# Kernel optimization log

Measured on AMD Instinct MI355X. Metric: run time of the kernel, lower is better.

## Reference

```python
import jax, jax.numpy as jnp
import numpy as np

BN_EPS = 1e-5

def setup_inputs() -> dict:
    key = jax.random.key(0)
    ks = jax.random.split(key, 6)
    B, C, N = 8, 256, 4096
    da = C // 4
    return {
        "x": jax.random.normal(ks[0], (B, C, N), dtype=jnp.float32),
        "Wq": jax.random.normal(ks[1], (da, C), dtype=jnp.float32) * (C ** -0.5),
        "Wk": jax.random.normal(ks[2], (da, C), dtype=jnp.float32) * (C ** -0.5),
        "Wv": jax.random.normal(ks[3], (C, C), dtype=jnp.float32) * (C ** -0.5),
        "Wp": jax.random.normal(ks[4], (C, C), dtype=jnp.float32) * (C ** -0.5),
        "bn_gamma": jnp.ones((C,), dtype=jnp.float32),
        "bn_beta": jnp.zeros((C,), dtype=jnp.float32),
        "bn_mean": jnp.zeros((C,), dtype=jnp.float32),
        "bn_var": jnp.ones((C,), dtype=jnp.float32),
    }

def reference(x, Wq, Wk, Wv, Wp, bn_gamma, bn_beta, bn_mean, bn_var):
    # x: [B, C, N]; 1x1 Conv1d == channel matmul
    q = jnp.einsum('bcn,dc->bnd', x, Wq)          # [B, N, da]
    k = jnp.einsum('bcn,dc->bdn', x, Wk)          # [B, da, N]
    v = jnp.einsum('bcn,dc->bnd', x, Wv)          # [B, N, C]
    energy = jnp.einsum('bnd,bdm->bnm', q, k)     # [B, N, N]
    # offset-attention double normalization: softmax over dim=1 (rows), then L1 over dim=-1
    attn = jax.nn.softmax(energy, axis=1)
    attn = attn / (1e-9 + attn.sum(axis=-1, keepdims=True))
    fsa = jnp.einsum('bnm,bmc->bcn', attn, v)     # [B, C, N]
    y = x - fsa
    h = jnp.einsum('bcn,dc->bdn', y, Wp)          # 1x1 conv of LBR
    # BatchNorm1d (inference-mode with running stats)
    inv = bn_gamma / jnp.sqrt(bn_var + BN_EPS)
    h = h * inv[None, :, None] + (bn_beta - bn_mean * inv)[None, :, None]
    return jax.nn.relu(h) + x
```

## Files before the change

### kernel.cpp

```cpp
#include <hip/hip_runtime.h>
#include <math.h>

#define BD 8
#define CD 256
#define ND 4096
#define DA 64

typedef __attribute__((ext_vector_type(8))) short short8v;
typedef __attribute__((ext_vector_type(4))) float float4v;

static __device__ __forceinline__ float4v mfma16(short8v a, short8v b, float4v c) {
  return __builtin_amdgcn_mfma_f32_16x16x32_bf16(a, b, c, 0, 0, 0);
}
static __device__ __forceinline__ unsigned short f2bf(float f) {
  union { float f; unsigned int u; } v; v.f = f;
  return (unsigned short)((v.u + 0x7fffu + ((v.u >> 16) & 1u)) >> 16);
}
static __device__ __forceinline__ float bf2f(unsigned short h) {
  union { unsigned int u; float f; } v; v.u = (unsigned int)h << 16;
  return v.f;
}
static __device__ __forceinline__ int sw(int row, int c8) {
  return row * 64 + (((c8) ^ (row & 7)) << 3);
}
typedef const __attribute__((address_space(1))) unsigned int g_u32;
typedef __attribute__((address_space(3))) unsigned int l_u32;
static __device__ __forceinline__ void gld16(const void* g, void* l) {
  __builtin_amdgcn_global_load_lds((g_u32*)g, (l_u32*)l, 16, 0, 0);
}

__global__ __launch_bounds__(256) void k_prep(const float* __restrict__ x,
                                              unsigned short* __restrict__ xTh,
                                              unsigned short* __restrict__ xTl) {
  const int n0 = blockIdx.x * 64, c0 = blockIdx.y * 64, b = blockIdx.z;
  __shared__ float Xs[64][68];
  const int tid = threadIdx.x;
  const int r0 = tid >> 4, col4 = (tid & 15) * 4;
#pragma unroll
  for (int j = 0; j < 4; ++j) {
    int r = r0 + j * 16;
    *(float4*)&Xs[r][col4] =
        *(const float4*)&x[((size_t)(b * CD + c0 + r)) * ND + n0 + col4];
  }
  __syncthreads();
  const int n = tid >> 2, cg = (tid & 3) * 16;
  unsigned short h[16], l[16];
#pragma unroll
  for (int j = 0; j < 16; ++j) {
    float v = Xs[cg + j][n];
    h[j] = f2bf(v);
    l[j] = f2bf(v - bf2f(h[j]));
  }
  size_t o = ((size_t)b * ND + n0 + n) * CD + c0 + cg;
#pragma unroll
  for (int j = 0; j < 4; ++j) {
    *(ushort4*)&xTh[o + j * 4] = *(ushort4*)&h[j * 4];
    *(ushort4*)&xTl[o + j * 4] = *(ushort4*)&l[j * 4];
  }
}

__global__ void k_prepW(const float* __restrict__ Wq, const float* __restrict__ Wk,
                        const float* __restrict__ Wv, const float* __restrict__ Wp,
                        unsigned short* Wch, unsigned short* Wcl,
                        unsigned short* Wph, unsigned short* Wpl) {
  int i = blockIdx.x * 256 + threadIdx.x;
  int row = i >> 6, c4 = (i & 63) * 4;
  const float* src; unsigned short *dh, *dl; int r, drow;
  if (row < 64)       { src = Wq; r = row;       dh = Wch; dl = Wcl; drow = row; }
  else if (row < 128) { src = Wk; r = row - 64;  dh = Wch; dl = Wcl; drow = row; }
  else if (row < 384) { src = Wv; r = row - 128; dh = Wch; dl = Wcl; drow = row; }
  else                { src = Wp; r = row - 384; dh = Wph; dl = Wpl; drow = row - 384; }
  float4 f = *(const float4*)&src[(size_t)r * 256 + c4];
  ushort4 hh, ll;
  hh.x = f2bf(f.x); hh.y = f2bf(f.y); hh.z = f2bf(f.z); hh.w = f2bf(f.w);
  ll.x = f2bf(f.x - bf2f(hh.x)); ll.y = f2bf(f.y - bf2f(hh.y));
  ll.z = f2bf(f.z - bf2f(hh.z)); ll.w = f2bf(f.w - bf2f(hh.w));
  *(ushort4*)&dh[(size_t)drow * 256 + c4] = hh;
  *(ushort4*)&dl[(size_t)drow * 256 + c4] = ll;
}

__global__ __launch_bounds__(512) void k_proj(
    const unsigned short* __restrict__ xTh, const unsigned short* __restrict__ xTl,
    const unsigned short* __restrict__ Wch, const unsigned short* __restrict__ Wcl,
    unsigned short* __restrict__ qh, unsigned short* __restrict__ kh,
    unsigned short* __restrict__ kl, unsigned short* __restrict__ vT) {
  const int n0 = blockIdx.x * 128, b = blockIdx.y;
  const int tid = threadIdx.x, w = tid >> 6, lane = tid & 63, lq = lane & 15,
            quad = lane >> 4;
  __shared__ __align__(16) unsigned short xs[2][2][128][40];
  float4v O[24];
#pragma unroll
  for (int t = 0; t < 24; ++t) O[t] = (float4v){0.f, 0.f, 0.f, 0.f};

  const int srow = tid >> 2, sc4 = tid & 3;
  uint4 rh, rl;
  auto load_slice = [&](int ks) {
    size_t a = ((size_t)b * ND + n0 + srow) * CD + ks * 32 + sc4 * 8;
    rh = *(const uint4*)(xTh + a);
    rl = *(const uint4*)(xTl + a);
  };
  auto write_slice = [&](int buf) {
    *(uint4*)&xs[buf][0][srow][sc4 * 8] = rh;
    *(uint4*)&xs[buf][1][srow][sc4 * 8] = rl;
  };
  load_slice(0); write_slice(0);
#pragma unroll 1
  for (int ks = 0; ks < 8; ++ks) {
    __syncthreads();
    if (ks < 7) load_slice(ks + 1);
    short8v bxh = *(const short8v*)&xs[ks & 1][0][w * 16 + lq][quad * 8];
    short8v bxl = *(const short8v*)&xs[ks & 1][1][w * 16 + lq][quad * 8];
#pragma unroll
    for (int t = 0; t < 24; ++t) {
      size_t a = (size_t)(t * 16 + lq) * CD + ks * 32 + quad * 8;
      short8v awh = *(const short8v*)(Wch + a);
      short8v awl = *(const short8v*)(Wcl + a);
      O[t] = mfma16(awh, bxh, O[t]);
      O[t] = mfma16(awl, bxh, O[t]);
      O[t] = mfma16(awh, bxl, O[t]);
    }
    if (ks < 7) write_slice((ks + 1) & 1);
  }
  const int n = n0 + w * 16 + lq;
#pragma unroll
  for (int t = 0; t < 24; ++t) {
    if (t < 4) {
      ushort4 hh;
      hh.x = f2bf(O[t][0]); hh.y = f2bf(O[t][1]);
      hh.z = f2bf(O[t][2]); hh.w = f2bf(O[t][3]);
      *(ushort4*)&qh[((size_t)b * ND + n) * DA + t * 16 + quad * 4] = hh;
    } else if (t < 8) {
      ushort4 hh, ll;
      hh.x = f2bf(O[t][0]); hh.y = f2bf(O[t][1]);
      hh.z = f2bf(O[t][2]); hh.w = f2bf(O[t][3]);
      ll.x = f2bf(O[t][0] - bf2f(hh.x)); ll.y = f2bf(O[t][1] - bf2f(hh.y));
      ll.z = f2bf(O[t][2] - bf2f(hh.z)); ll.w = f2bf(O[t][3] - bf2f(hh.w));
      size_t o = ((size_t)b * ND + n) * DA + (t - 4) * 16 + quad * 4;
      *(ushort4*)&kh[o] = hh;
      *(ushort4*)&kl[o] = ll;
    } else {
#pragma unroll
      for (int r = 0; r < 4; ++r) {
        int c = (t - 8) * 16 + quad * 4 + r;
        vT[((size_t)b * CD + c) * ND + n] = f2bf(O[t][r]);
      }
    }
  }
}

__global__ __launch_bounds__(512, 4) void k_colsum(
    const unsigned short* __restrict__ qh, const unsigned short* __restrict__ khp,
    const unsigned short* __restrict__ klp, float* __restrict__ Dp) {
  const int bid = blockIdx.x, b = bid & 7, half = (bid >> 3) & 1,
            m0 = (bid >> 4) * 128;
  const int nbase = half * 2048;
  const int tid = threadIdx.x, w = tid >> 6, lane = tid & 63, lq = lane & 15,
            quad = lane >> 4;
  const int mq = w & 3, nh = w >> 2;
  __shared__ __align__(16) unsigned short qbuf[3][4096];
  __shared__ float Cb[128];
  short8v bkh[2][2], bkl[2][2];
#pragma unroll
  for (int sub = 0; sub < 2; ++sub)
#pragma unroll
    for (int k = 0; k < 2; ++k) {
      size_t a = ((size_t)b * ND + m0 + mq * 32 + sub * 16 + lq) * DA + k * 32 + quad * 8;
      bkh[sub][k] = *(const short8v*)(khp + a);
      bkl[sub][k] = *(const short8v*)(klp + a);
    }
  const int srow = w * 8 + (lane >> 3), sck = lane & 7;
  auto stageQ = [&](int it, int qn) {
    const unsigned short* src = qh + ((size_t)b * ND + nbase + it * 64 + srow) * DA +
                                ((sck ^ (srow & 7)) << 3);
    gld16(src, &qbuf[qn][0] + (size_t)w * 512);
  };
  stageQ(0, 0);
  stageQ(1, 1);
  asm volatile("s_waitcnt vmcnt(1)\n\ts_barrier" ::: "memory");
  float cs0 = 0.f, cs1 = 0.f;
  int rc = 0, sc = 2;
#pragma unroll 1
  for (int i = 0; i < 32; ++i) {
    if (i < 30) { stageQ(i + 2, sc); sc = (sc + 1 == 3) ? 0 : sc + 1; }
#pragma unroll
    for (int s = 0; s < 2; ++s) {
      short8v ah[2];
#pragma unroll
      for (int k = 0; k < 2; ++k)
        ah[k] = *(const short8v*)&qbuf[rc][sw(nh * 32 + s * 16 + lq, k * 4 + quad)];
#pragma unroll
      for (int sub = 0; sub < 2; ++sub) {
        float4v acc = {0.f, 0.f, 0.f, 0.f};
#pragma unroll
        for (int k = 0; k < 2; ++k) {
          acc = mfma16(ah[k], bkh[sub][k], acc);
          acc = mfma16(ah[k], bkl[sub][k], acc);
        }
        float e0 = __expf(acc[0]) + __expf(acc[1]) + __expf(acc[2]) + __expf(acc[3]);
        if (sub == 0) cs0 += e0; else cs1 += e0;
      }
    }
    rc = (rc + 1 == 3) ? 0 : rc + 1;
    if (i < 30)
      asm volatile("s_waitcnt vmcnt(1) lgkmcnt(0)\n\ts_barrier" ::: "memory");
    else
      asm volatile("s_waitcnt vmcnt(0) lgkmcnt(0)\n\ts_barrier" ::: "memory");
  }
  cs0 += __shfl_down(cs0, 16); cs0 += __shfl_down(cs0, 32);
  cs1 += __shfl_down(cs1, 16); cs1 += __shfl_down(cs1, 32);
  if (nh == 0 && lane < 16) {
    Cb[mq * 32 + lane] = cs0;
    Cb[mq * 32 + 16 + lane] = cs1;
  }
  __syncthreads();
  if (nh == 1 && lane < 16) {
    float t0 = Cb[mq * 32 + lane] + cs0;
    float t1 = Cb[mq * 32 + 16 + lane] + cs1;
    size_t o = (size_t)half * (BD * ND) + (size_t)b * ND + m0 + mq * 32 + lane;
    Dp[o] = t0;
    Dp[o + 16] = t1;
  }
}

__global__ void k_rcp(const float* __restrict__ Dp, float* __restrict__ Drec) {
  int i = blockIdx.x * 256 + threadIdx.x;
  float4 a = *(const float4*)&Dp[(size_t)i * 4];
  float4 c = *(const float4*)&Dp[(size_t)(BD * ND) + (size_t)i * 4];
  float4 r;
  r.x = 1.f / (a.x + c.x); r.y = 1.f / (a.y + c.y);
  r.z = 1.f / (a.z + c.z); r.w = 1.f / (a.w + c.w);
  *(float4*)&Drec[(size_t)i * 4] = r;
}

__global__ __launch_bounds__(512, 2) void k_attn(
    const unsigned short* __restrict__ qh, const unsigned short* __restrict__ khp,
    const unsigned short* __restrict__ klp, const unsigned short* __restrict__ vT,
    const float* __restrict__ Drec, unsigned short* xhy,
    const unsigned short* __restrict__ xTl) {
  const int bid = blockIdx.x, b = bid & 7, n0 = (bid >> 3) * 128;
  const int tid = threadIdx.x, w = tid >> 6, lane = tid & 63, lq = lane & 15,
            quad = lane >> 4;
  const int nq = w & 3, ch = w >> 2;
  __shared__ __align__(16) unsigned short vbuf[3][16384];
  __shared__ __align__(16) unsigned short Pb[2][8192];
  __shared__ float Sb[128];

  short8v aq[2][2];
#pragma unroll
  for (int s = 0; s < 2; ++s)
#pragma unroll
    for (int k = 0; k < 2; ++k)
      aq[s][k] = *(const short8v*)(qh + ((size_t)b * ND + n0 + nq * 32 + s * 16 + lq) * DA +
                                   k * 32 + quad * 8);
  float4v O[2][8];
#pragma unroll
  for (int s = 0; s < 2; ++s)
#pragma unroll
    for (int t = 0; t < 8; ++t) O[s][t] = (float4v){0.f, 0.f, 0.f, 0.f};
  float rs[2] = {0.f, 0.f};

  auto stageV = [&](int mt, int vn) {
    unsigned short* base = &vbuf[vn][0];
#pragma unroll
    for (int j = 0; j < 4; ++j) {
      int cidx = tid + j * 512;
      int row = cidx >> 3, ckpos = cidx & 7;
      const unsigned short* src =
          vT + ((size_t)b * CD + row) * ND + mt * 64 + ((ckpos ^ (row & 7)) << 3);
      gld16(src, base + (size_t)(w * 64 + j * 512) * 8);
    }
  };
  short8v kc[8], kn[8];
  auto kload = [&](short8v* dst, int mt) {
#pragma unroll
    for (int sub = 0; sub < 2; ++sub)
#pragma unroll
      for (int k = 0; k < 2; ++k) {
        size_t a = ((size_t)b * ND + mt * 64 + ch * 32 + sub * 16 + lq) * DA +
                   k * 32 + quad * 8;
        dst[sub * 4 + k * 2 + 0] = *(const short8v*)(khp + a);
        dst[sub * 4 + k * 2 + 1] = *(const short8v*)(klp + a);
      }
  };
  auto doPV = [&](const unsigned short* Pc, const unsigned short* vc) {
    short8v ap[2][2];
#pragma unroll
    for (int s = 0; s < 2; ++s)
#pragma unroll
      for (int k = 0; k < 2; ++k)
        ap[s][k] = *(const short8v*)&Pc[sw(nq * 32 + s * 16 + lq, k * 4 + quad)];
#pragma unroll
    for (int t = 0; t < 8; ++t) {
      const int trow = (ch * 8 + t) * 16 + lq;
#pragma unroll
      for (int k = 0; k < 2; ++k) {
        short8v bv = *(const short8v*)&vc[sw(trow, k * 4 + quad)];
#pragma unroll
        for (int s = 0; s < 2; ++s) O[s][t] = mfma16(bv, ap[s][k], O[s][t]);
      }
    }
  };

  float4 drc4[2], drn4[2];
  stageV(0, 0);
  kload(kc, 0);
#pragma unroll
  for (int sub = 0; sub < 2; ++sub)
    drc4[sub] = *(const float4*)&Drec[(size_t)b * ND + ch * 32 + sub * 16 + quad * 4];

  int vs = 1, vp = 0;
#pragma unroll 1
  for (int i = 0; i < 64; ++i) {
    if (i > 0) {
      doPV(&Pb[(i - 1) & 1][0], &vbuf[vp][0]);
      vp = (vp + 1 == 3) ? 0 : vp + 1;
    }
    if (i < 63) {
      kload(kn, i + 1);
#pragma unroll
      for (int sub = 0; sub < 2; ++sub)
        drn4[sub] = *(const float4*)&Drec[(size_t)b * ND + (i + 1) * 64 + ch * 32 +
                                          sub * 16 + quad * 4];
      stageV(i + 1, vs);
      vs = (vs + 1 == 3) ? 0 : vs + 1;
    }
    unsigned short* Pcur = &Pb[i & 1][0];
#pragma unroll
    for (int sub = 0; sub < 2; ++sub) {
#pragma unroll
      for (int s = 0; s < 2; ++s) {
        float4v acc = {0.f, 0.f, 0.f, 0.f};
#pragma unroll
        for (int k = 0; k < 2; ++k) {
          acc = mfma16(kc[sub * 4 + k * 2 + 0], aq[s][k], acc);
          acc = mfma16(kc[sub * 4 + k * 2 + 1], aq[s][k], acc);
        }
        float p0 = __expf(acc[0]) * drc4[sub].x;
        float p1 = __expf(acc[1]) * drc4[sub].y;
        float p2 = __expf(acc[2]) * drc4[sub].z;
        float p3 = __expf(acc[3]) * drc4[sub].w;
        rs[s] += (p0 + p1) + (p2 + p3);
        unsigned int w0 =
            (__float_as_uint(p0) >> 16) | (__float_as_uint(p1) & 0xffff0000u);
        unsigned int w1 =
            (__float_as_uint(p2) >> 16) | (__float_as_uint(p3) & 0xffff0000u);
        const int nl = nq * 32 + s * 16 + lq;
        const int c8 = ch * 4 + sub * 2 + (quad >> 1);
        uint2 wv; wv.x = w0; wv.y = w1;
        *(uint2*)&Pcur[nl * 64 + ((c8 ^ (nl & 7)) << 3) + ((quad & 1) << 2)] = wv;
      }
    }
    if (i < 63) {
#pragma unroll
      for (int t = 0; t < 8; ++t) kc[t] = kn[t];
      drc4[0] = drn4[0]; drc4[1] = drn4[1];
    }
    if (i < 63)
      asm volatile("s_waitcnt vmcnt(4) lgkmcnt(0)\n\ts_barrier" ::: "memory");
    else
      asm volatile("s_waitcnt vmcnt(0) lgkmcnt(0)\n\ts_barrier" ::: "memory");
  }
  doPV(&Pb[1][0], &vbuf[vp][0]);

  rs[0] += __shfl_xor(rs[0], 16); rs[0] += __shfl_xor(rs[0], 32);
  rs[1] += __shfl_xor(rs[1], 16); rs[1] += __shfl_xor(rs[1], 32);
  if (ch == 0 && lane < 16) {
    Sb[nq * 32 + lane] = rs[0];
    Sb[nq * 32 + 16 + lane] = rs[1];
  }
  __syncthreads();
  if (ch == 1 && lane < 16) {
    Sb[nq * 32 + lane] += rs[0];
    Sb[nq * 32 + 16 + lane] += rs[1];
  }
  __syncthreads();
  float rsc[2];
#pragma unroll
  for (int s = 0; s < 2; ++s)
    rsc[s] = 1.0f / (1e-9f + Sb[nq * 32 + s * 16 + lq]);
#pragma unroll
  for (int t = 0; t < 8; ++t) {
    const int cb = (ch * 8 + t) * 16 + quad * 4;
#pragma unroll
    for (int s = 0; s < 2; ++s) {
      const int n = n0 + nq * 32 + s * 16 + lq;
      const size_t off = ((size_t)b * ND + n) * CD + cb;
      ushort4 h4 = *(const ushort4*)&xhy[off];
      ushort4 l4 = *(const ushort4*)&xTl[off];
      ushort4 o4;
      o4.x = f2bf(bf2f(h4.x) + bf2f(l4.x) - O[s][t][0] * rsc[s]);
      o4.y = f2bf(bf2f(h4.y) + bf2f(l4.y) - O[s][t][1] * rsc[s]);
      o4.z = f2bf(bf2f(h4.z) + bf2f(l4.z) - O[s][t][2] * rsc[s]);
      o4.w = f2bf(bf2f(h4.w) + bf2f(l4.w) - O[s][t][3] * rsc[s]);
      *(ushort4*)&xhy[off] = o4;
    }
  }
}

__global__ __launch_bounds__(256) void k_final(const unsigned short* __restrict__ y,
                                               const unsigned short* __restrict__ Wpb,
                                               const float* __restrict__ x,
                                               const float* __restrict__ gamma,
                                               const float* __restrict__ beta,
                                               const float* __restrict__ mean,
                                               const float* __restrict__ var,
                                               float* __restrict__ out) {
  const int bid = blockIdx.x;
  const int b = bid & 7;
  const int rem = bid >> 3;
  const int n0 = (rem & 63) * 64;
  const int d0 = (rem >> 6) * 64;
  const int tid = threadIdx.x;
  const int wave = tid >> 6, lane = tid & 63, lq = lane & 15, quad = lane >> 4;
  const int dw = d0 + wave * 16;
  float4v O[4];
#pragma unroll
  for (int s = 0; s < 4; ++s) O[s] = (float4v){0.f, 0.f, 0.f, 0.f};
#pragma unroll
  for (int chh = 0; chh < 8; ++chh) {
    const size_t ab = (size_t)(dw + lq) * CD + chh * 32 + quad * 8;
    short8v a0 = *(const short8v*)(Wpb + ab);
#pragma unroll
    for (int s = 0; s < 4; ++s) {
      const size_t bb = ((size_t)b * ND + n0 + s * 16 + lq) * CD + chh * 32 + quad * 8;
      short8v bv = *(const short8v*)(y + bb);
      O[s] = mfma16(a0, bv, O[s]);
    }
  }
#pragma unroll
  for (int r = 0; r < 4; ++r) {
    const int d = dw + quad * 4 + r;
    const float inv  = gamma[d] / sqrtf(var[d] + 1e-5f);
    const float bias = beta[d] - mean[d] * inv;
#pragma unroll
    for (int s = 0; s < 4; ++s) {
      const int n = n0 + s * 16 + lq;
      const size_t oi = ((size_t)b * CD + d) * ND + n;
      out[oi] = fmaxf(O[s][r] * inv + bias, 0.f) + x[oi];
    }
  }
}

extern "C" void kernel_launch(void* const* d_in, const int* in_sizes, int n_in,
                              void* d_out, int out_size, void* d_ws, size_t ws_size,
                              hipStream_t stream) {
  const float* x     = (const float*)d_in[0];
  const float* Wq    = (const float*)d_in[1];
  const float* Wk    = (const float*)d_in[2];
  const float* Wv    = (const float*)d_in[3];
  const float* Wp    = (const float*)d_in[4];
  const float* gamma = (const float*)d_in[5];
  const float* beta  = (const float*)d_in[6];
  const float* mean  = (const float*)d_in[7];
  const float* var   = (const float*)d_in[8];
  float* out = (float*)d_out;

  char* wsp = (char*)d_ws;
  unsigned short* qhp = (unsigned short*)wsp; wsp += (size_t)BD * ND * DA * 2;
  unsigned short* khp = (unsigned short*)wsp; wsp += (size_t)BD * ND * DA * 2;
  unsigned short* klp = (unsigned short*)wsp; wsp += (size_t)BD * ND * DA * 2;
  unsigned short* vT  = (unsigned short*)wsp; wsp += (size_t)BD * CD * ND * 2;
  unsigned short* xTh = (unsigned short*)wsp; wsp += (size_t)BD * ND * CD * 2;
  unsigned short* xTl = (unsigned short*)wsp; wsp += (size_t)BD * ND * CD * 2;
  unsigned short* Wch = (unsigned short*)wsp; wsp += (size_t)384 * 256 * 2;
  unsigned short* Wcl = (unsigned short*)wsp; wsp += (size_t)384 * 256 * 2;
  unsigned short* Wph = (unsigned short*)wsp; wsp += (size_t)256 * 256 * 2;
  unsigned short* Wpl = (unsigned short*)wsp; wsp += (size_t)256 * 256 * 2;
  float* Drec = (float*)wsp; wsp += (size_t)BD * ND * 4;
  float* Dp   = (float*)wsp; wsp += (size_t)2 * BD * ND * 4;
  unsigned short* y = xTh;

  dim3 blk(256), blk5(512);
  k_prep<<<dim3(ND / 64, CD / 64, BD), blk, 0, stream>>>(x, xTh, xTl);
  k_prepW<<<dim3(160), blk, 0, stream>>>(Wq, Wk, Wv, Wp, Wch, Wcl, Wph, Wpl);
  k_proj<<<dim3(ND / 128, BD), blk5, 0, stream>>>(xTh, xTl, Wch, Wcl, qhp, khp,
                                                  klp, vT);
  k_colsum<<<dim3(512), blk5, 0, stream>>>(qhp, khp, klp, Dp);
  k_rcp<<<dim3(32), blk, 0, stream>>>(Dp, Drec);
  k_attn<<<dim3(256), blk5, 0, stream>>>(qhp, khp, klp, vT, Drec, y, xTl);
  k_final<<<dim3(2048), blk, 0, stream>>>(y, Wph, x, gamma, beta, mean, var, out);
}
```

Measured before the change: 512.0 us.

## Materialize exp-energy matrix in halves and run separate PV GEMM

The old code computed the energy matrix twice: once for column sums and once inside the fused attention kernel. The new code computes exp(energy) once per half of the key dimension and stores it as a bf16 P matrix in global memory, writing column sums at the same time. A second pass takes reciprocals of those column sums and folds them into V in place. A separate GEMM kernel then computes P·V and the row sums, and accumulates partial results across the two halves through an fp32 buffer. This removes the recomputed QK products but adds a large write and read of P through HBM, plus extra kernel launches.

```diff
diff --git a/kernel.cpp b/kernel.cpp
--- a/kernel.cpp
+++ b/kernel.cpp
@@ -5,6 +5,8 @@
 #define CD 256
 #define ND 4096
 #define DA 64
+#define HM 2048
+#define OSTR 260
 
 typedef __attribute__((ext_vector_type(8))) short short8v;
 typedef __attribute__((ext_vector_type(4))) float float4v;
@@ -148,16 +150,19 @@
   }
 }
 
-__global__ __launch_bounds__(512, 4) void k_colsum(
+__global__ __launch_bounds__(512, 4) void k_expE(
     const unsigned short* __restrict__ qh, const unsigned short* __restrict__ khp,
-    const unsigned short* __restrict__ klp, float* __restrict__ Dp) {
-  const int bid = blockIdx.x, b = bid & 7, half = (bid >> 3) & 1,
-            m0 = (bid >> 4) * 128;
-  const int nbase = half * 2048;
+    const unsigned short* __restrict__ klp, unsigned short* __restrict__ P,
+    float* __restrict__ Dp, int mhalf) {
+  const int mtile = blockIdx.x, nq4 = blockIdx.y, b = blockIdx.z;
+  const int m0 = mhalf * HM + mtile * 128;
+  const int mmb = mtile * 128;
+  const int nbase = nq4 * 1024;
   const int tid = threadIdx.x, w = tid >> 6, lane = tid & 63, lq = lane & 15,
             quad = lane >> 4;
   const int mq = w & 3, nh = w >> 2;
-  __shared__ __align__(16) unsigned short qbuf[3][4096];
+  __shared__ __align__(16) unsigned short qbuf[2][4096];
+  __shared__ __align__(16) unsigned short Et[64][136];
   __shared__ float Cb[128];
   short8v bkh[2][2], bkl[2][2];
 #pragma unroll
@@ -168,232 +173,262 @@
       bkh[sub][k] = *(const short8v*)(khp + a);
       bkl[sub][k] = *(const short8v*)(klp + a);
     }
-  const int srow = w * 8 + (lane >> 3), sck = lane & 7;
-  auto stageQ = [&](int it, int qn) {
+  const int srow = tid >> 3, sck = tid & 7;
+  auto stageQ = [&](int it, int buf) {
     const unsigned short* src = qh + ((size_t)b * ND + nbase + it * 64 + srow) * DA +
                                 ((sck ^ (srow & 7)) << 3);
-    gld16(src, &qbuf[qn][0] + (size_t)w * 512);
+    gld16(src, &qbuf[buf][0] + (size_t)w * 512);
   };
+  float cs[2][4] = {{0.f, 0.f, 0.f, 0.f}, {0.f, 0.f, 0.f, 0.f}};
   stageQ(0, 0);
-  stageQ(1, 1);
-  asm volatile("s_waitcnt vmcnt(1)\n\ts_barrier" ::: "memory");
-  float cs0 = 0.f, cs1 = 0.f;
-  int rc = 0, sc = 2;
+  asm volatile("s_waitcnt vmcnt(0)\n\ts_barrier" ::: "memory");
 #pragma unroll 1
-  for (int i = 0; i < 32; ++i) {
-    if (i < 30) { stageQ(i + 2, sc); sc = (sc + 1 == 3) ? 0 : sc + 1; }
+  for (int i = 0; i < 16; ++i) {
+    if (i < 15) stageQ(i + 1, (i + 1) & 1);
 #pragma unroll
     for (int s = 0; s < 2; ++s) {
       short8v ah[2];
 #pragma unroll
       for (int k = 0; k < 2; ++k)
-        ah[k] = *(const short8v*)&qbuf[rc][sw(nh * 32 + s * 16 + lq, k * 4 + quad)];
+        ah[k] = *(const short8v*)&qbuf[i & 1][sw(nh * 32 + s * 16 + lq, k * 4 + quad)];
 #pragma unroll
       for (int sub = 0; sub < 2; ++sub) {
         float4v acc = {0.f, 0.f, 0.f, 0.f};
 #pragma unroll
         for (int k = 0; k < 2; ++k) {
-          acc = mfma16(ah[k], bkh[sub][k], acc);
-          acc = mfma16(ah[k], bkl[sub][k], acc);
+          acc = mfma16(bkh[sub][k], ah[k], acc);
+          acc = mfma16(bkl[sub][k], ah[k], acc);
         }
-        float e0 = __expf(acc[0]) + __expf(acc[1]) + __expf(acc[2]) + __expf(acc[3]);
-        if (sub == 0) cs0 += e0; else cs1 += e0;
-      }
-    }
-    rc = (rc + 1 == 3) ? 0 : rc + 1;
-    if (i < 30)
-      asm volatile("s_waitcnt vmcnt(1) lgkmcnt(0)\n\ts_barrier" ::: "memory");
-    else
-      asm volatile("s_waitcnt vmcnt(0) lgkmcnt(0)\n\ts_barrier" ::: "memory");
-  }
-  cs0 += __shfl_down(cs0, 16); cs0 += __shfl_down(cs0, 32);
-  cs1 += __shfl_down(cs1, 16); cs1 += __shfl_down(cs1, 32);
-  if (nh == 0 && lane < 16) {
-    Cb[mq * 32 + lane] = cs0;
-    Cb[mq * 32 + 16 + lane] = cs1;
-  }
-  __syncthreads();
-  if (nh == 1 && lane < 16) {
-    float t0 = Cb[mq * 32 + lane] + cs0;
-    float t1 = Cb[mq * 32 + 16 + lane] + cs1;
-    size_t o = (size_t)half * (BD * ND) + (size_t)b * ND + m0 + mq * 32 + lane;
-    Dp[o] = t0;
-    Dp[o + 16] = t1;
-  }
-}
-
-__global__ void k_rcp(const float* __restrict__ Dp, float* __restrict__ Drec) {
-  int i = blockIdx.x * 256 + threadIdx.x;
-  float4 a = *(const float4*)&Dp[(size_t)i * 4];
-  float4 c = *(const float4*)&Dp[(size_t)(BD * ND) + (size_t)i * 4];
-  float4 r;
-  r.x = 1.f / (a.x + c.x); r.y = 1.f / (a.y + c.y);
-  r.z = 1.f / (a.z + c.z); r.w = 1.f / (a.w + c.w);
-  *(float4*)&Drec[(size_t)i * 4] = r;
-}
-
-__global__ __launch_bounds__(512, 2) void k_attn(
-    const unsigned short* __restrict__ qh, const unsigned short* __restrict__ khp,
-    const unsigned short* __restrict__ klp, const unsigned short* __restrict__ vT,
-    const float* __restrict__ Drec, unsigned short* xhy,
-    const unsigned short* __restrict__ xTl) {
-  const int bid = blockIdx.x, b = bid & 7, n0 = (bid >> 3) * 128;
-  const int tid = threadIdx.x, w = tid >> 6, lane = tid & 63, lq = lane & 15,
-            quad = lane >> 4;
-  const int nq = w & 3, ch = w >> 2;
-  __shared__ __align__(16) unsigned short vbuf[3][16384];
-  __shared__ __align__(16) unsigned short Pb[2][8192];
-  __shared__ float Sb[128];
-
-  short8v aq[2][2];
-#pragma unroll
-  for (int s = 0; s < 2; ++s)
-#pragma unroll
-    for (int k = 0; k < 2; ++k)
-      aq[s][k] = *(const short8v*)(qh + ((size_t)b * ND + n0 + nq * 32 + s * 16 + lq) * DA +
-                                   k * 32 + quad * 8);
-  float4v O[2][8];
-#pragma unroll
-  for (int s = 0; s < 2; ++s)
-#pragma unroll
-    for (int t = 0; t < 8; ++t) O[s][t] = (float4v){0.f, 0.f, 0.f, 0.f};
-  float rs[2] = {0.f, 0.f};
-
-  auto stageV = [&](int mt, int vn) {
-    unsigned short* base = &vbuf[vn][0];
-#pragma unroll
-    for (int j = 0; j < 4; ++j) {
-      int cidx = tid + j * 512;
-      int row = cidx >> 3, ckpos = cidx & 7;
-      const unsigned short* src =
-          vT + ((size_t)b * CD + row) * ND + mt * 64 + ((ckpos ^ (row & 7)) << 3);
-      gld16(src, base + (size_t)(w * 64 + j * 512) * 8);
-    }
-  };
-  short8v kc[8], kn[8];
-  auto kload = [&](short8v* dst, int mt) {
-#pragma unroll
-    for (int sub = 0; sub < 2; ++sub)
-#pragma unroll
-      for (int k = 0; k < 2; ++k) {
-        size_t a = ((size_t)b * ND + mt * 64 + ch * 32 + sub * 16 + lq) * DA +
-                   k * 32 + quad * 8;
-        dst[sub * 4 + k * 2 + 0] = *(const short8v*)(khp + a);
-        dst[sub * 4 + k * 2 + 1] = *(const short8v*)(klp + a);
-      }
-  };
-  auto doPV = [&](const unsigned short* Pc, const unsigned short* vc) {
-    short8v ap[2][2];
-#pragma unroll
-    for (int s = 0; s < 2; ++s)
-#pragma unroll
-      for (int k = 0; k < 2; ++k)
-        ap[s][k] = *(const short8v*)&Pc[sw(nq * 32 + s * 16 + lq, k * 4 + quad)];
-#pragma unroll
-    for (int t = 0; t < 8; ++t) {
-      const int trow = (ch * 8 + t) * 16 + lq;
-#pragma unroll
-      for (int k = 0; k < 2; ++k) {
-        short8v bv = *(const short8v*)&vc[sw(trow, k * 4 + quad)];
-#pragma unroll
-        for (int s = 0; s < 2; ++s) O[s][t] = mfma16(bv, ap[s][k], O[s][t]);
-      }
-    }
-  };
-
-  float4 drc4[2], drn4[2];
-  stageV(0, 0);
-  kload(kc, 0);
-#pragma unroll
-  for (int sub = 0; sub < 2; ++sub)
-    drc4[sub] = *(const float4*)&Drec[(size_t)b * ND + ch * 32 + sub * 16 + quad * 4];
-
-  int vs = 1, vp = 0;
-#pragma unroll 1
-  for (int i = 0; i < 64; ++i) {
-    if (i > 0) {
-      doPV(&Pb[(i - 1) & 1][0], &vbuf[vp][0]);
-      vp = (vp + 1 == 3) ? 0 : vp + 1;
-    }
-    if (i < 63) {
-      kload(kn, i + 1);
-#pragma unroll
-      for (int sub = 0; sub < 2; ++sub)
-        drn4[sub] = *(const float4*)&Drec[(size_t)b * ND + (i + 1) * 64 + ch * 32 +
-                                          sub * 16 + quad * 4];
-      stageV(i + 1, vs);
-      vs = (vs + 1 == 3) ? 0 : vs + 1;
-    }
-    unsigned short* Pcur = &Pb[i & 1][0];
-#pragma unroll
-    for (int sub = 0; sub < 2; ++sub) {
-#pragma unroll
-      for (int s = 0; s < 2; ++s) {
-        float4v acc = {0.f, 0.f, 0.f, 0.f};
-#pragma unroll
-        for (int k = 0; k < 2; ++k) {
-          acc = mfma16(kc[sub * 4 + k * 2 + 0], aq[s][k], acc);
-          acc = mfma16(kc[sub * 4 + k * 2 + 1], aq[s][k], acc);
-        }
-        float p0 = __expf(acc[0]) * drc4[sub].x;
-        float p1 = __expf(acc[1]) * drc4[sub].y;
-        float p2 = __expf(acc[2]) * drc4[sub].z;
-        float p3 = __expf(acc[3]) * drc4[sub].w;
-        rs[s] += (p0 + p1) + (p2 + p3);
+        float p0 = __expf(acc[0]), p1 = __expf(acc[1]);
+        float p2 = __expf(acc[2]), p3 = __expf(acc[3]);
+        cs[sub][0] += p0; cs[sub][1] += p1; cs[sub][2] += p2; cs[sub][3] += p3;
         unsigned int w0 =
             (__float_as_uint(p0) >> 16) | (__float_as_uint(p1) & 0xffff0000u);
         unsigned int w1 =
             (__float_as_uint(p2) >> 16) | (__float_as_uint(p3) & 0xffff0000u);
-        const int nl = nq * 32 + s * 16 + lq;
-        const int c8 = ch * 4 + sub * 2 + (quad >> 1);
+        const int nl = nh * 32 + s * 16 + lq;
         uint2 wv; wv.x = w0; wv.y = w1;
-        *(uint2*)&Pcur[nl * 64 + ((c8 ^ (nl & 7)) << 3) + ((quad & 1) << 2)] = wv;
+        *(uint2*)((unsigned short*)Et + nl * 136 + mq * 32 + sub * 16 + quad * 4) = wv;
       }
     }
-    if (i < 63) {
-#pragma unroll
-      for (int t = 0; t < 8; ++t) kc[t] = kn[t];
-      drc4[0] = drn4[0]; drc4[1] = drn4[1];
-    }
-    if (i < 63)
-      asm volatile("s_waitcnt vmcnt(4) lgkmcnt(0)\n\ts_barrier" ::: "memory");
-    else
-      asm volatile("s_waitcnt vmcnt(0) lgkmcnt(0)\n\ts_barrier" ::: "memory");
-  }
-  doPV(&Pb[1][0], &vbuf[vp][0]);
-
-  rs[0] += __shfl_xor(rs[0], 16); rs[0] += __shfl_xor(rs[0], 32);
-  rs[1] += __shfl_xor(rs[1], 16); rs[1] += __shfl_xor(rs[1], 32);
-  if (ch == 0 && lane < 16) {
-    Sb[nq * 32 + lane] = rs[0];
-    Sb[nq * 32 + 16 + lane] = rs[1];
+    asm volatile("s_waitcnt lgkmcnt(0)\n\ts_barrier" ::: "memory");
+    {
+      uint4 u0 = *(const uint4*)((const unsigned short*)Et + srow * 136 + sck * 16);
+      uint4 u1 = *(const uint4*)((const unsigned short*)Et + srow * 136 + sck * 16 + 8);
+      size_t po = ((size_t)b * ND + nbase + i * 64 + srow) * HM + mmb + sck * 16;
+      *(uint4*)(P + po) = u0;
+      *(uint4*)(P + po + 8) = u1;
+    }
+    asm volatile("s_waitcnt vmcnt(2) lgkmcnt(0)\n\ts_barrier" ::: "memory");
+  }
+#pragma unroll
+  for (int sub = 0; sub < 2; ++sub)
+#pragma unroll
+    for (int r = 0; r < 4; ++r) {
+      cs[sub][r] += __shfl_xor(cs[sub][r], 1);
+      cs[sub][r] += __shfl_xor(cs[sub][r], 2);
+      cs[sub][r] += __shfl_xor(cs[sub][r], 4);
+      cs[sub][r] += __shfl_xor(cs[sub][r], 8);
+    }
+  if (nh == 0 && lq == 0) {
+#pragma unroll
+    for (int sub = 0; sub < 2; ++sub) {
+      float4 v4; v4.x = cs[sub][0]; v4.y = cs[sub][1]; v4.z = cs[sub][2]; v4.w = cs[sub][3];
+      *(float4*)&Cb[mq * 32 + sub * 16 + quad * 4] = v4;
+    }
   }
   __syncthreads();
-  if (ch == 1 && lane < 16) {
-    Sb[nq * 32 + lane] += rs[0];
-    Sb[nq * 32 + 16 + lane] += rs[1];
-  }
-  __syncthreads();
-  float rsc[2];
-#pragma unroll
-  for (int s = 0; s < 2; ++s)
-    rsc[s] = 1.0f / (1e-9f + Sb[nq * 32 + s * 16 + lq]);
-#pragma unroll
-  for (int t = 0; t < 8; ++t) {
-    const int cb = (ch * 8 + t) * 16 + quad * 4;
-#pragma unroll
-    for (int s = 0; s < 2; ++s) {
-      const int n = n0 + nq * 32 + s * 16 + lq;
-      const size_t off = ((size_t)b * ND + n) * CD + cb;
-      ushort4 h4 = *(const ushort4*)&xhy[off];
-      ushort4 l4 = *(const ushort4*)&xTl[off];
-      ushort4 o4;
-      o4.x = f2bf(bf2f(h4.x) + bf2f(l4.x) - O[s][t][0] * rsc[s]);
-      o4.y = f2bf(bf2f(h4.y) + bf2f(l4.y) - O[s][t][1] * rsc[s]);
-      o4.z = f2bf(bf2f(h4.z) + bf2f(l4.z) - O[s][t][2] * rsc[s]);
-      o4.w = f2bf(bf2f(h4.w) + bf2f(l4.w) - O[s][t][3] * rsc[s]);
-      *(ushort4*)&xhy[off] = o4;
-    }
+  if (nh == 1 && lq == 0) {
+#pragma unroll
+    for (int sub = 0; sub < 2; ++sub) {
+      float4 v4 = *(const float4*)&Cb[mq * 32 + sub * 16 + quad * 4];
+      v4.x += cs[sub][0]; v4.y += cs[sub][1]; v4.z += cs[sub][2]; v4.w += cs[sub][3];
+      *(float4*)&Dp[((size_t)nq4 * 8 + b) * HM + mmb + mq * 32 + sub * 16 + quad * 4] = v4;
+    }
+  }
+}
+
+__global__ void k_rcp2(const float* __restrict__ Dp, float* __restrict__ drc,
+                       int mhalf) {
+  int i = blockIdx.x * 256 + threadIdx.x;
+  int b = i >> 9, mm = (i & 511) * 4;
+  float4 s0 = *(const float4*)&Dp[((size_t)0 * 8 + b) * HM + mm];
+  float4 s1 = *(const float4*)&Dp[((size_t)1 * 8 + b) * HM + mm];
+  float4 s2 = *(const float4*)&Dp[((size_t)2 * 8 + b) * HM + mm];
+  float4 s3 = *(const float4*)&Dp[((size_t)3 * 8 + b) * HM + mm];
+  float4 r;
+  r.x = 1.f / (s0.x + s1.x + s2.x + s3.x);
+  r.y = 1.f / (s0.y + s1.y + s2.y + s3.y);
+  r.z = 1.f / (s0.z + s1.z + s2.z + s3.z);
+  r.w = 1.f / (s0.w + s1.w + s2.w + s3.w);
+  *(float4*)&drc[(size_t)b * ND + mhalf * HM + mm] = r;
+}
+
+__global__ void k_vext(unsigned short* __restrict__ vT,
+                       const float* __restrict__ drc, int mhalf) {
+  int idx = blockIdx.x * 256 + threadIdx.x;
+  int m8 = idx & 255, c = (idx >> 8) & 255, b = idx >> 16;
+  const int mb = mhalf * HM + m8 * 8;
+  size_t va = ((size_t)(b * CD + c)) * ND + mb;
+  short8v v = *(const short8v*)(vT + va);
+  float4 d0 = *(const float4*)&drc[(size_t)b * ND + mb];
+  float4 d1 = *(const float4*)&drc[(size_t)b * ND + mb + 4];
+  ushort4 o0, o1;
+  o0.x = f2bf(bf2f((unsigned short)v[0]) * d0.x);
+  o0.y = f2bf(bf2f((unsigned short)v[1]) * d0.y);
+  o0.z = f2bf(bf2f((unsigned short)v[2]) * d0.z);
+  o0.w = f2bf(bf2f((unsigned short)v[3]) * d0.w);
+  o1.x = f2bf(bf2f((unsigned short)v[4]) * d1.x);
+  o1.y = f2bf(bf2f((unsigned short)v[5]) * d1.y);
+  o1.z = f2bf(bf2f((unsigned short)v[6]) * d1.z);
+  o1.w = f2bf(bf2f((unsigned short)v[7]) * d1.w);
+  *(ushort4*)(vT + va) = o0;
+  *(ushort4*)(vT + va + 4) = o1;
+}
+
+__global__ __launch_bounds__(512, 2) void k_pv(
+    const unsigned short* __restrict__ P, const unsigned short* __restrict__ vext,
+    const float* __restrict__ drc, float* __restrict__ Oa,
+    unsigned short* __restrict__ xhy, const unsigned short* __restrict__ xTl,
+    int mhalf, int last) {
+  const int n0 = blockIdx.x * 128, b = blockIdx.y;
+  const int tid = threadIdx.x, w = tid >> 6, lane = tid & 63, lq = lane & 15,
+            quad = lane >> 4;
+  const int wc = w & 3, wn = w >> 2;
+  __shared__ __align__(16) unsigned short pbuf[3][8192];
+  __shared__ float Sb[128];
+  float4v O[4][4];
+#pragma unroll
+  for (int tc = 0; tc < 4; ++tc)
+#pragma unroll
+    for (int tn = 0; tn < 4; ++tn) O[tc][tn] = (float4v){0.f, 0.f, 0.f, 0.f};
+  float rs = 0.f;
+
+  short8v ac[8], an[8];
+  auto aload = [&](short8v* d, int mm) {
+#pragma unroll
+    for (int tc = 0; tc < 4; ++tc)
+#pragma unroll
+      for (int s32 = 0; s32 < 2; ++s32)
+        d[tc * 2 + s32] = *(const short8v*)(
+            vext + ((size_t)(b * CD) + wc * 64 + tc * 16 + lq) * ND + mhalf * HM +
+            mm + s32 * 32 + quad * 8);
+  };
+  float4 dc[4], dn[4];
+  auto dload = [&](float4* d, int mm) {
+#pragma unroll
+    for (int s32 = 0; s32 < 2; ++s32) {
+      size_t a = (size_t)b * ND + mhalf * HM + mm + s32 * 32 + quad * 8;
+      d[s32 * 2] = *(const float4*)(drc + a);
+      d[s32 * 2 + 1] = *(const float4*)(drc + a + 4);
+    }
+  };
+  auto stageP = [&](int mt, int vn) {
+    unsigned short* base = &pbuf[vn][0];
+#pragma unroll
+    for (int j = 0; j < 2; ++j) {
+      int cidx = tid + j * 512;
+      int row = cidx >> 3, ck = cidx & 7;
+      const unsigned short* src = P + ((size_t)b * ND + n0 + row) * HM + mt * 64 +
+                                  ((ck ^ (row & 7)) << 3);
+      gld16(src, base + (size_t)(w * 64 + j * 512) * 8);
+    }
+  };
+
+  aload(ac, 0);
+  dload(dc, 0);
+  stageP(0, 0);
+  stageP(1, 1);
+  asm volatile("s_waitcnt vmcnt(2)\n\ts_barrier" ::: "memory");
+
+  int rc = 0, vs = 2;
+#pragma unroll 1
+  for (int i = 0; i < 32; ++i) {
+    if (i < 31) {
+      aload(an, (i + 1) * 64);
+      dload(dn, (i + 1) * 64);
+    }
+    if (i < 30) {
+      stageP(i + 2, vs);
+      vs = (vs + 1 == 3) ? 0 : vs + 1;
+    }
+#pragma unroll
+    for (int s32 = 0; s32 < 2; ++s32) {
+      short8v bp[4];
+#pragma unroll
+      for (int tn = 0; tn < 4; ++tn) {
+        bp[tn] = *(const short8v*)&pbuf[rc][sw(wn * 64 + tn * 16 + lq, s32 * 4 + quad)];
+        if (tn == wc) {
+          float4 da = dc[s32 * 2], db = dc[s32 * 2 + 1];
+          rs += bf2f((unsigned short)bp[tn][0]) * da.x;
+          rs += bf2f((unsigned short)bp[tn][1]) * da.y;
+          rs += bf2f((unsigned short)bp[tn][2]) * da.z;
+          rs += bf2f((unsigned short)bp[tn][3]) * da.w;
+          rs += bf2f((unsigned short)bp[tn][4]) * db.x;
+          rs += bf2f((unsigned short)bp[tn][5]) * db.y;
+          rs += bf2f((unsigned short)bp[tn][6]) * db.z;
+          rs += bf2f((unsigned short)bp[tn][7]) * db.w;
+        }
+      }
+#pragma unroll
+      for (int tc = 0; tc < 4; ++tc)
+#pragma unroll
+        for (int tn = 0; tn < 4; ++tn)
+          O[tc][tn] = mfma16(ac[tc * 2 + s32], bp[tn], O[tc][tn]);
+    }
+    if (i < 31) {
+#pragma unroll
+      for (int t = 0; t < 8; ++t) ac[t] = an[t];
+#pragma unroll
+      for (int t = 0; t < 4; ++t) dc[t] = dn[t];
+    }
+    rc = (rc + 1 == 3) ? 0 : rc + 1;
+    if (i < 30)
+      asm volatile("s_waitcnt vmcnt(2) lgkmcnt(0)\n\ts_barrier" ::: "memory");
+    else if (i == 30)
+      asm volatile("s_waitcnt vmcnt(12) lgkmcnt(0)\n\ts_barrier" ::: "memory");
+  }
+
+  rs += __shfl_xor(rs, 16);
+  rs += __shfl_xor(rs, 32);
+  if (!last) {
+#pragma unroll
+    for (int tc = 0; tc < 4; ++tc)
+#pragma unroll
+      for (int tn = 0; tn < 4; ++tn) {
+        const int n = n0 + wn * 64 + tn * 16 + lq, c = wc * 64 + tc * 16 + quad * 4;
+        float4 v4;
+        v4.x = O[tc][tn][0]; v4.y = O[tc][tn][1];
+        v4.z = O[tc][tn][2]; v4.w = O[tc][tn][3];
+        *(float4*)&Oa[((size_t)b * ND + n) * OSTR + c] = v4;
+      }
+    if (quad == 0)
+      Oa[((size_t)b * ND + n0 + wn * 64 + wc * 16 + lq) * OSTR + 256] = rs;
+  } else {
+    if (quad == 0)
+      Sb[wn * 64 + wc * 16 + lq] =
+          rs + Oa[((size_t)b * ND + n0 + wn * 64 + wc * 16 + lq) * OSTR + 256];
+    __syncthreads();
+    float rsc[4];
+#pragma unroll
+    for (int tn = 0; tn < 4; ++tn)
+      rsc[tn] = 1.0f / (1e-9f + Sb[wn * 64 + tn * 16 + lq]);
+#pragma unroll
+    for (int tc = 0; tc < 4; ++tc)
+#pragma unroll
+      for (int tn = 0; tn < 4; ++tn) {
+        const int n = n0 + wn * 64 + tn * 16 + lq, c = wc * 64 + tc * 16 + quad * 4;
+        float4 po = *(const float4*)&Oa[((size_t)b * ND + n) * OSTR + c];
+        const size_t off = ((size_t)b * ND + n) * CD + c;
+        ushort4 h4 = *(const ushort4*)&xhy[off];
+        ushort4 l4 = *(const ushort4*)&xTl[off];
+        ushort4 o4;
+        o4.x = f2bf(bf2f(h4.x) + bf2f(l4.x) - (O[tc][tn][0] + po.x) * rsc[tn]);
+        o4.y = f2bf(bf2f(h4.y) + bf2f(l4.y) - (O[tc][tn][1] + po.y) * rsc[tn]);
+        o4.z = f2bf(bf2f(h4.z) + bf2f(l4.z) - (O[tc][tn][2] + po.z) * rsc[tn]);
+        o4.w = f2bf(bf2f(h4.w) + bf2f(l4.w) - (O[tc][tn][3] + po.w) * rsc[tn]);
+        *(ushort4*)&xhy[off] = o4;
+      }
   }
 }
 
@@ -466,8 +501,10 @@
   unsigned short* Wcl = (unsigned short*)wsp; wsp += (size_t)384 * 256 * 2;
   unsigned short* Wph = (unsigned short*)wsp; wsp += (size_t)256 * 256 * 2;
   unsigned short* Wpl = (unsigned short*)wsp; wsp += (size_t)256 * 256 * 2;
-  float* Drec = (float*)wsp; wsp += (size_t)BD * ND * 4;
-  float* Dp   = (float*)wsp; wsp += (size_t)2 * BD * ND * 4;
+  float* drc = (float*)wsp; wsp += (size_t)BD * ND * 4;
+  float* Dp  = (float*)wsp; wsp += (size_t)4 * BD * HM * 4;
+  float* Oa  = (float*)wsp; wsp += (size_t)BD * ND * OSTR * 4;
+  unsigned short* P = (unsigned short*)wsp; wsp += (size_t)BD * ND * HM * 2;
   unsigned short* y = xTh;
 
   dim3 blk(256), blk5(512);
@@ -475,8 +512,11 @@
   k_prepW<<<dim3(160), blk, 0, stream>>>(Wq, Wk, Wv, Wp, Wch, Wcl, Wph, Wpl);
   k_proj<<<dim3(ND / 128, BD), blk5, 0, stream>>>(xTh, xTl, Wch, Wcl, qhp, khp,
                                                   klp, vT);
-  k_colsum<<<dim3(512), blk5, 0, stream>>>(qhp, khp, klp, Dp);
-  k_rcp<<<dim3(32), blk, 0, stream>>>(Dp, Drec);
-  k_attn<<<dim3(256), blk5, 0, stream>>>(qhp, khp, klp, vT, Drec, y, xTl);
+  for (int h = 0; h < 2; ++h) {
+    k_expE<<<dim3(16, 4, BD), blk5, 0, stream>>>(qhp, khp, klp, P, Dp, h);
+    k_rcp2<<<dim3(16), blk, 0, stream>>>(Dp, drc, h);
+    k_vext<<<dim3(2048), blk, 0, stream>>>(vT, drc, h);
+    k_pv<<<dim3(32, BD), blk5, 0, stream>>>(P, vT, drc, Oa, y, xTl, h, h);
+  }
   k_final<<<dim3(2048), blk, 0, stream>>>(y, Wph, x, gamma, beta, mean, var, out);
 }
```

After: 563.7 us. 10.1% more time.

## Split attention work across 16 waves per block instead of 8

Applied to the files above, without the earlier changes.

The attention kernel now runs 1024 threads per block, with four channel-quarter wave groups instead of two. Each wave computes a 16-key slice of the energy tile and a quarter of the output channels, which halves per-wave accumulators and staging work. The row sums are reduced through a four-way shared buffer. The aim is more waves to hide latency and lower register pressure, at the cost of more barrier participants and a launch bound of 1024 threads with 4 blocks requested per CU, which shared memory may not support.

```diff
diff --git a/kernel.cpp b/kernel.cpp
--- a/kernel.cpp
+++ b/kernel.cpp
@@ -232,7 +232,7 @@
   *(float4*)&Drec[(size_t)i * 4] = r;
 }
 
-__global__ __launch_bounds__(512, 2) void k_attn(
+__global__ __launch_bounds__(1024, 4) void k_attn(
     const unsigned short* __restrict__ qh, const unsigned short* __restrict__ khp,
     const unsigned short* __restrict__ klp, const unsigned short* __restrict__ vT,
     const float* __restrict__ Drec, unsigned short* xhy,
@@ -240,10 +240,10 @@
   const int bid = blockIdx.x, b = bid & 7, n0 = (bid >> 3) * 128;
   const int tid = threadIdx.x, w = tid >> 6, lane = tid & 63, lq = lane & 15,
             quad = lane >> 4;
-  const int nq = w & 3, ch = w >> 2;
+  const int nq = w & 3, cq = w >> 2;
   __shared__ __align__(16) unsigned short vbuf[3][16384];
   __shared__ __align__(16) unsigned short Pb[2][8192];
-  __shared__ float Sb[128];
+  __shared__ float Sb4[4][128];
 
   short8v aq[2][2];
 #pragma unroll
@@ -252,35 +252,32 @@
     for (int k = 0; k < 2; ++k)
       aq[s][k] = *(const short8v*)(qh + ((size_t)b * ND + n0 + nq * 32 + s * 16 + lq) * DA +
                                    k * 32 + quad * 8);
-  float4v O[2][8];
+  float4v O[2][4];
 #pragma unroll
   for (int s = 0; s < 2; ++s)
 #pragma unroll
-    for (int t = 0; t < 8; ++t) O[s][t] = (float4v){0.f, 0.f, 0.f, 0.f};
+    for (int t = 0; t < 4; ++t) O[s][t] = (float4v){0.f, 0.f, 0.f, 0.f};
   float rs[2] = {0.f, 0.f};
 
   auto stageV = [&](int mt, int vn) {
     unsigned short* base = &vbuf[vn][0];
 #pragma unroll
-    for (int j = 0; j < 4; ++j) {
-      int cidx = tid + j * 512;
+    for (int j = 0; j < 2; ++j) {
+      int cidx = tid + j * 1024;
       int row = cidx >> 3, ckpos = cidx & 7;
       const unsigned short* src =
           vT + ((size_t)b * CD + row) * ND + mt * 64 + ((ckpos ^ (row & 7)) << 3);
-      gld16(src, base + (size_t)(w * 64 + j * 512) * 8);
-    }
-  };
-  short8v kc[8], kn[8];
+      gld16(src, base + (size_t)(w * 64 + j * 1024) * 8);
+    }
+  };
+  short8v kc[4], kn[4];
   auto kload = [&](short8v* dst, int mt) {
 #pragma unroll
-    for (int sub = 0; sub < 2; ++sub)
-#pragma unroll
-      for (int k = 0; k < 2; ++k) {
-        size_t a = ((size_t)b * ND + mt * 64 + ch * 32 + sub * 16 + lq) * DA +
-                   k * 32 + quad * 8;
-        dst[sub * 4 + k * 2 + 0] = *(const short8v*)(khp + a);
-        dst[sub * 4 + k * 2 + 1] = *(const short8v*)(klp + a);
-      }
+    for (int k = 0; k < 2; ++k) {
+      size_t a = ((size_t)b * ND + mt * 64 + cq * 16 + lq) * DA + k * 32 + quad * 8;
+      dst[k * 2 + 0] = *(const short8v*)(khp + a);
+      dst[k * 2 + 1] = *(const short8v*)(klp + a);
+    }
   };
   auto doPV = [&](const unsigned short* Pc, const unsigned short* vc) {
     short8v ap[2][2];
@@ -290,8 +287,8 @@
       for (int k = 0; k < 2; ++k)
         ap[s][k] = *(const short8v*)&Pc[sw(nq * 32 + s * 16 + lq, k * 4 + quad)];
 #pragma unroll
-    for (int t = 0; t < 8; ++t) {
-      const int trow = (ch * 8 + t) * 16 + lq;
+    for (int t = 0; t < 4; ++t) {
+      const int trow = (cq * 4 + t) * 16 + lq;
 #pragma unroll
       for (int k = 0; k < 2; ++k) {
         short8v bv = *(const short8v*)&vc[sw(trow, k * 4 + quad)];
@@ -301,12 +298,10 @@
     }
   };
 
-  float4 drc4[2], drn4[2];
+  float4 drc4, drn4;
   stageV(0, 0);
   kload(kc, 0);
-#pragma unroll
-  for (int sub = 0; sub < 2; ++sub)
-    drc4[sub] = *(const float4*)&Drec[(size_t)b * ND + ch * 32 + sub * 16 + quad * 4];
+  drc4 = *(const float4*)&Drec[(size_t)b * ND + cq * 16 + quad * 4];
 
   int vs = 1, vp = 0;
 #pragma unroll 1
@@ -317,46 +312,40 @@
     }
     if (i < 63) {
       kload(kn, i + 1);
-#pragma unroll
-      for (int sub = 0; sub < 2; ++sub)
-        drn4[sub] = *(const float4*)&Drec[(size_t)b * ND + (i + 1) * 64 + ch * 32 +
-                                          sub * 16 + quad * 4];
+      drn4 = *(const float4*)&Drec[(size_t)b * ND + (i + 1) * 64 + cq * 16 + quad * 4];
       stageV(i + 1, vs);
       vs = (vs + 1 == 3) ? 0 : vs + 1;
     }
     unsigned short* Pcur = &Pb[i & 1][0];
 #pragma unroll
-    for (int sub = 0; sub < 2; ++sub) {
-#pragma unroll
-      for (int s = 0; s < 2; ++s) {
-        float4v acc = {0.f, 0.f, 0.f, 0.f};
-#pragma unroll
-        for (int k = 0; k < 2; ++k) {
-          acc = mfma16(kc[sub * 4 + k * 2 + 0], aq[s][k], acc);
-          acc = mfma16(kc[sub * 4 + k * 2 + 1], aq[s][k], acc);
-        }
-        float p0 = __expf(acc[0]) * drc4[sub].x;
-        float p1 = __expf(acc[1]) * drc4[sub].y;
-        float p2 = __expf(acc[2]) * drc4[sub].z;
-        float p3 = __expf(acc[3]) * drc4[sub].w;
-        rs[s] += (p0 + p1) + (p2 + p3);
-        unsigned int w0 =
-            (__float_as_uint(p0) >> 16) | (__float_as_uint(p1) & 0xffff0000u);
-        unsigned int w1 =
-            (__float_as_uint(p2) >> 16) | (__float_as_uint(p3) & 0xffff0000u);
-        const int nl = nq * 32 + s * 16 + lq;
-        const int c8 = ch * 4 + sub * 2 + (quad >> 1);
-        uint2 wv; wv.x = w0; wv.y = w1;
-        *(uint2*)&Pcur[nl * 64 + ((c8 ^ (nl & 7)) << 3) + ((quad & 1) << 2)] = wv;
+    for (int s = 0; s < 2; ++s) {
+      float4v acc = {0.f, 0.f, 0.f, 0.f};
+#pragma unroll
+      for (int k = 0; k < 2; ++k) {
+        acc = mfma16(kc[k * 2 + 0], aq[s][k], acc);
+        acc = mfma16(kc[k * 2 + 1], aq[s][k], acc);
       }
+      float p0 = __expf(acc[0]) * drc4.x;
+      float p1 = __expf(acc[1]) * drc4.y;
+      float p2 = __expf(acc[2]) * drc4.z;
+      float p3 = __expf(acc[3]) * drc4.w;
+      rs[s] += (p0 + p1) + (p2 + p3);
+      unsigned int w0 =
+          (__float_as_uint(p0) >> 16) | (__float_as_uint(p1) & 0xffff0000u);
+      unsigned int w1 =
+          (__float_as_uint(p2) >> 16) | (__float_as_uint(p3) & 0xffff0000u);
+      const int nl = nq * 32 + s * 16 + lq;
+      const int c8 = cq * 2 + (quad >> 1);
+      uint2 wv; wv.x = w0; wv.y = w1;
+      *(uint2*)&Pcur[nl * 64 + ((c8 ^ (nl & 7)) << 3) + ((quad & 1) << 2)] = wv;
     }
     if (i < 63) {
 #pragma unroll
-      for (int t = 0; t < 8; ++t) kc[t] = kn[t];
-      drc4[0] = drn4[0]; drc4[1] = drn4[1];
+      for (int t = 0; t < 4; ++t) kc[t] = kn[t];
+      drc4 = drn4;
     }
     if (i < 63)
-      asm volatile("s_waitcnt vmcnt(4) lgkmcnt(0)\n\ts_barrier" ::: "memory");
+      asm volatile("s_waitcnt vmcnt(2) lgkmcnt(0)\n\ts_barrier" ::: "memory");
     else
       asm volatile("s_waitcnt vmcnt(0) lgkmcnt(0)\n\ts_barrier" ::: "memory");
   }
@@ -364,23 +353,20 @@
 
   rs[0] += __shfl_xor(rs[0], 16); rs[0] += __shfl_xor(rs[0], 32);
   rs[1] += __shfl_xor(rs[1], 16); rs[1] += __shfl_xor(rs[1], 32);
-  if (ch == 0 && lane < 16) {
-    Sb[nq * 32 + lane] = rs[0];
-    Sb[nq * 32 + 16 + lane] = rs[1];
-  }
-  __syncthreads();
-  if (ch == 1 && lane < 16) {
-    Sb[nq * 32 + lane] += rs[0];
-    Sb[nq * 32 + 16 + lane] += rs[1];
+  if (lane < 16) {
+    Sb4[cq][nq * 32 + lane] = rs[0];
+    Sb4[cq][nq * 32 + 16 + lane] = rs[1];
   }
   __syncthreads();
   float rsc[2];
 #pragma unroll
-  for (int s = 0; s < 2; ++s)
-    rsc[s] = 1.0f / (1e-9f + Sb[nq * 32 + s * 16 + lq]);
-#pragma unroll
-  for (int t = 0; t < 8; ++t) {
-    const int cb = (ch * 8 + t) * 16 + quad * 4;
+  for (int s = 0; s < 2; ++s) {
+    const int nloc = nq * 32 + s * 16 + lq;
+    rsc[s] = 1.0f / (1e-9f + Sb4[0][nloc] + Sb4[1][nloc] + Sb4[2][nloc] + Sb4[3][nloc]);
+  }
+#pragma unroll
+  for (int t = 0; t < 4; ++t) {
+    const int cb = (cq * 4 + t) * 16 + quad * 4;
 #pragma unroll
     for (int s = 0; s < 2; ++s) {
       const int n = n0 + nq * 32 + s * 16 + lq;
@@ -470,13 +456,13 @@
   float* Dp   = (float*)wsp; wsp += (size_t)2 * BD * ND * 4;
   unsigned short* y = xTh;
 
-  dim3 blk(256), blk5(512);
+  dim3 blk(256), blk5(512), blkA(1024);
   k_prep<<<dim3(ND / 64, CD / 64, BD), blk, 0, stream>>>(x, xTh, xTl);
   k_prepW<<<dim3(160), blk, 0, stream>>>(Wq, Wk, Wv, Wp, Wch, Wcl, Wph, Wpl);
   k_proj<<<dim3(ND / 128, BD), blk5, 0, stream>>>(xTh, xTl, Wch, Wcl, qhp, khp,
                                                   klp, vT);
   k_colsum<<<dim3(512), blk5, 0, stream>>>(qhp, khp, klp, Dp);
   k_rcp<<<dim3(32), blk, 0, stream>>>(Dp, Drec);
-  k_attn<<<dim3(256), blk5, 0, stream>>>(qhp, khp, klp, vT, Drec, y, xTl);
+  k_attn<<<dim3(256), blkA, 0, stream>>>(qhp, khp, klp, vT, Drec, y, xTl);
   k_final<<<dim3(2048), blk, 0, stream>>>(y, Wph, x, gamma, beta, mean, var, out);
 }
```

Result: faster. 492.3 us (-3.8%).
